# Performance work log

Measured on AMD Instinct MI355X. Metric: run time of the kernel, lower is better.

## Reference

```python
import jax, jax.numpy as jnp
import numpy as np

L, B, T, C = 4, 4, 2048, 1024
FFN = 4 * C
STD = 0.02
EPS = 1e-5
NEG_INF = -1e38


def setup_inputs() -> dict:
    key = jax.random.key(0)
    ks = jax.random.split(key, 18)
    n = lambda k, shape, s=STD: jax.random.normal(k, shape, jnp.float32) * s
    u = lambda k, shape: jax.random.uniform(k, shape, jnp.float32)
    return {
        "x": jax.random.normal(ks[0], (B, T, C), jnp.float32),
        "ln1_w": jnp.ones((L, C), jnp.float32),
        "tm_mix_k": u(ks[1], (L, 1, 1, C)),
        "tm_mix_v": u(ks[2], (L, 1, 1, C)),
        "tm_mix_r": u(ks[3], (L, 1, 1, C)),
        "tm_k_w": n(ks[4], (L, C, C)),
        "tm_v_w": n(ks[5], (L, C, C)),
        "tm_r_w": n(ks[6], (L, C, C)),
        "tm_o_w": n(ks[7], (L, C, C)),
        # time_decay in [-5, 1] like RWKV decay_speed init; w = -exp(time_decay)
        "time_decay": u(ks[8], (L, C)) * 6.0 - 5.0,
        "time_first": jnp.log(0.3).astype(jnp.float32) + 0.5 * jax.random.normal(ks[9], (L, C), jnp.float32),
        "ln2_w": jnp.ones((L, C), jnp.float32),
        "cm_mix_k": u(ks[10], (L, 1, 1, C)),
        "cm_mix_r": u(ks[11], (L, 1, 1, C)),
        "cm_k_w": n(ks[12], (L, FFN, C)),
        "cm_v_w": n(ks[13], (L, C, FFN)),
        "cm_r_w": n(ks[14], (L, C, C)),
        "lnf_w": jnp.ones((C,), jnp.float32),
    }


def layer_norm(x, w):
    mu = jnp.mean(x, axis=-1, keepdims=True)
    var = jnp.mean(jnp.square(x - mu), axis=-1, keepdims=True)
    return (x - mu) * jax.lax.rsqrt(var + EPS) * w


def time_shift(x):
    # ZeroPad2d((0,0,1,-1)): shift sequence right by one, zero at t=0
    return jnp.pad(x, ((0, 0), (1, 0), (0, 0)))[:, :-1]


def wkv_scan(k, v, time_decay, time_first):
    # k, v: [B, T, C]; numerically-stabilized linear WKV recurrence over T
    w = -jnp.exp(time_decay)  # [C]
    u = time_first            # [C]
    zeros = jnp.zeros(k.shape[::2], k.dtype)  # [B, C]

    def step(carry, kv):
        num, den, mx = carry
        kt, vt = kv
        max_out = jnp.maximum(mx, kt + u)
        e1 = jnp.exp(mx - max_out)
        e2 = jnp.exp(kt + u - max_out)
        out = (e1 * num + e2 * vt) / (e1 * den + e2)
        max_st = jnp.maximum(mx + w, kt)
        e1 = jnp.exp(mx + w - max_st)
        e2 = jnp.exp(kt - max_st)
        return (e1 * num + e2 * vt, e1 * den + e2, max_st), out

    init = (zeros, zeros, jnp.full_like(zeros, NEG_INF))
    _, out = jax.lax.scan(step, init, (k.swapaxes(0, 1), v.swapaxes(0, 1)))
    return out.swapaxes(0, 1)  # [B, T, C]


def reference(x, ln1_w, tm_mix_k, tm_mix_v, tm_mix_r, tm_k_w, tm_v_w, tm_r_w, tm_o_w,
              time_decay, time_first, ln2_w, cm_mix_k, cm_mix_r, cm_k_w, cm_v_w, cm_r_w, lnf_w):
    n_layer = ln1_w.shape[0]
    for l in range(n_layer):
        # --- TimeMixing ---
        h = layer_norm(x, ln1_w[l])
        prev = time_shift(h)
        k = jnp.einsum('btc,oc->bto', h * tm_mix_k[l] + prev * (1 - tm_mix_k[l]), tm_k_w[l])
        v = jnp.einsum('btc,oc->bto', h * tm_mix_v[l] + prev * (1 - tm_mix_v[l]), tm_v_w[l])
        r = jax.nn.sigmoid(jnp.einsum('btc,oc->bto', h * tm_mix_r[l] + prev * (1 - tm_mix_r[l]), tm_r_w[l]))
        wkv = wkv_scan(k, v, time_decay[l], time_first[l])
        x = x + jnp.einsum('btc,oc->bto', r * wkv, tm_o_w[l])
        # --- ChannelMixing ---
        h = layer_norm(x, ln2_w[l])
        prev = time_shift(h)
        kk = jnp.einsum('btc,fc->btf', h * cm_mix_k[l] + prev * (1 - cm_mix_k[l]), cm_k_w[l])  # [B,T,4C]
        vv = jnp.einsum('btf,of->bto', jnp.square(jax.nn.relu(kk)), cm_v_w[l])
        rr = jax.nn.sigmoid(jnp.einsum('btc,oc->bto', h * cm_mix_r[l] + prev * (1 - cm_mix_r[l]), cm_r_w[l]))
        x = x + rr * vv
    return layer_norm(x, lnf_w)
```

## Files before the change

### kernel.cpp

```cpp
#include <hip/hip_runtime.h>
#include <hip/hip_bf16.h>


#define LNUM 4
#define BSZ  4
#define TSZ  2048
#define CSZ  1024
#define FFND 4096
#define MROWS (BSZ*TSZ)
#define EPSF 1e-5f

typedef __hip_bfloat16 bf16;
typedef __bf16 bf16x8 __attribute__((ext_vector_type(8)));
typedef float f32x4 __attribute__((ext_vector_type(4)));

#define BM 128
#define BK 64

#define SCK  64
#define SLEN (TSZ/SCK)

__device__ __forceinline__ void async_copy16(const void* g, void* l) {
    __builtin_amdgcn_global_load_lds((const __attribute__((address_space(1))) void*)g,
                                     (__attribute__((address_space(3))) void*)l, 16, 0, 0);
}

template<int MODE, int TBN>
__launch_bounds__(256)
__global__ void gemm_bt(const bf16* __restrict__ A, const bf16* __restrict__ Bw,
                        void* __restrict__ outp, const bf16* __restrict__ aux,
                        int K, int N)
{
    constexpr int MT  = (TBN == 128) ? 4 : 2;
    constexpr int NBI = TBN / 32;
    __shared__ __align__(16) __bf16 sA[BM*BK];
    __shared__ __align__(16) __bf16 sB[TBN*BK];
    const int tid  = threadIdx.x;
    const int lane = tid & 63;
    const int wid  = tid >> 6;
    const int wmB  = (TBN == 128) ? (wid >> 1) * 64 : wid * 32;
    const int wnB  = (TBN == 128) ? (wid & 1) * 64 : 0;
    const size_t bm0 = (size_t)blockIdx.x * BM;
    const size_t bn0 = (size_t)blockIdx.y * TBN;

    const int lrow8 = lane >> 3;
    const int cbg   = (lane & 7) ^ lrow8;

    const bf16* pA[4]; const bf16* pB[NBI];
#pragma unroll
    for (int i = 0; i < 4; ++i)
        pA[i] = A + (bm0 + (i*4 + wid)*8 + lrow8) * (size_t)K + cbg*8;
#pragma unroll
    for (int i = 0; i < NBI; ++i)
        pB[i] = Bw + (bn0 + (i*4 + wid)*8 + lrow8) * (size_t)K + cbg*8;

    f32x4 acc[MT][4];
#pragma unroll
    for (int a = 0; a < MT; ++a)
#pragma unroll
        for (int b = 0; b < 4; ++b) acc[a][b] = (f32x4){0.f,0.f,0.f,0.f};

    const int q   = lane >> 4;
    const int rlo = lane & 15;

    const int ktiles = K / BK;
    for (int kt = 0; kt < ktiles; ++kt) {
#pragma unroll
        for (int i = 0; i < 4; ++i) {
            async_copy16(pA[i], &sA[(i*4 + wid)*8*BK]);
            pA[i] += BK;
        }
#pragma unroll
        for (int i = 0; i < NBI; ++i) {
            async_copy16(pB[i], &sB[(i*4 + wid)*8*BK]);
            pB[i] += BK;
        }
        __syncthreads();
#pragma unroll
        for (int ks = 0; ks < 2; ++ks) {
            bf16x8 aF[MT], bF[4];
#pragma unroll
            for (int mt = 0; mt < MT; ++mt) {
                const int r  = wmB + mt*16 + rlo;
                const int cb = (ks*4 + q) ^ (r & 7);
                aF[mt] = *(const bf16x8*)&sA[r*BK + cb*8];
            }
#pragma unroll
            for (int nt = 0; nt < 4; ++nt) {
                const int r  = wnB + nt*16 + rlo;
                const int cb = (ks*4 + q) ^ (r & 7);
                bF[nt] = *(const bf16x8*)&sB[r*BK + cb*8];
            }
#pragma unroll
            for (int mt = 0; mt < MT; ++mt)
#pragma unroll
                for (int nt = 0; nt < 4; ++nt)
                    acc[mt][nt] = __builtin_amdgcn_mfma_f32_16x16x32_bf16(
                        aF[mt], bF[nt], acc[mt][nt], 0, 0, 0);
        }
        __syncthreads();
    }

#pragma unroll
    for (int mt = 0; mt < MT; ++mt) {
#pragma unroll
        for (int nt = 0; nt < 4; ++nt) {
            const size_t col = bn0 + wnB + nt*16 + rlo;
#pragma unroll
            for (int i = 0; i < 4; ++i) {
                const size_t row = bm0 + wmB + mt*16 + q*4 + i;
                const size_t idx = row * (size_t)N + col;
                const float v = acc[mt][nt][i];
                if (MODE == 2) {
                    ((float*)outp)[idx] += v;
                } else if (MODE == 3) {
                    const float t = fmaxf(v, 0.f);
                    ((bf16*)outp)[idx] = __float2bfloat16(t*t);
                } else if (MODE == 4) {
                    ((bf16*)outp)[idx] = __float2bfloat16(1.f/(1.f+__expf(-v)));
                } else if (MODE == 6) {
                    ((float*)outp)[idx] = ((const float*)aux)[idx] + v;
                } else {
                    ((float*)outp)[idx] += (float)aux[idx] * v;
                }
            }
        }
    }
}

__launch_bounds__(256)
__global__ void gemm_kvr(const bf16* __restrict__ A0, const bf16* __restrict__ A1,
                         const bf16* __restrict__ A2,
                         const bf16* __restrict__ W0, const bf16* __restrict__ W1,
                         const bf16* __restrict__ W2,
                         bf16* __restrict__ O0, bf16* __restrict__ O1,
                         bf16* __restrict__ O2)
{
    constexpr int TBN = 64, MT = 2, NBI = 2, K = CSZ, N = CSZ;
    const int z = blockIdx.z;
    const bf16* A  = (z == 0) ? A0 : (z == 1) ? A1 : A2;
    const bf16* Bw = (z == 0) ? W0 : (z == 1) ? W1 : W2;
    bf16* outp     = (z == 0) ? O0 : (z == 1) ? O1 : O2;

    __shared__ __align__(16) __bf16 sA[BM*BK];
    __shared__ __align__(16) __bf16 sB[TBN*BK];
    const int tid  = threadIdx.x;
    const int lane = tid & 63;
    const int wid  = tid >> 6;
    const int wmB  = wid * 32;
    const size_t bm0 = (size_t)blockIdx.x * BM;
    const size_t bn0 = (size_t)blockIdx.y * TBN;

    const int lrow8 = lane >> 3;
    const int cbg   = (lane & 7) ^ lrow8;

    const bf16* pA[4]; const bf16* pB[NBI];
#pragma unroll
    for (int i = 0; i < 4; ++i)
        pA[i] = A + (bm0 + (i*4 + wid)*8 + lrow8) * (size_t)K + cbg*8;
#pragma unroll
    for (int i = 0; i < NBI; ++i)
        pB[i] = Bw + (bn0 + (i*4 + wid)*8 + lrow8) * (size_t)K + cbg*8;

    f32x4 acc[MT][4];
#pragma unroll
    for (int a = 0; a < MT; ++a)
#pragma unroll
        for (int b = 0; b < 4; ++b) acc[a][b] = (f32x4){0.f,0.f,0.f,0.f};

    const int q   = lane >> 4;
    const int rlo = lane & 15;

    for (int kt = 0; kt < K/BK; ++kt) {
#pragma unroll
        for (int i = 0; i < 4; ++i) {
            async_copy16(pA[i], &sA[(i*4 + wid)*8*BK]);
            pA[i] += BK;
        }
#pragma unroll
        for (int i = 0; i < NBI; ++i) {
            async_copy16(pB[i], &sB[(i*4 + wid)*8*BK]);
            pB[i] += BK;
        }
        __syncthreads();
#pragma unroll
        for (int ks = 0; ks < 2; ++ks) {
            bf16x8 aF[MT], bF[4];
#pragma unroll
            for (int mt = 0; mt < MT; ++mt) {
                const int r  = wmB + mt*16 + rlo;
                const int cb = (ks*4 + q) ^ (r & 7);
                aF[mt] = *(const bf16x8*)&sA[r*BK + cb*8];
            }
#pragma unroll
            for (int nt = 0; nt < 4; ++nt) {
                const int r  = nt*16 + rlo;
                const int cb = (ks*4 + q) ^ (r & 7);
                bF[nt] = *(const bf16x8*)&sB[r*BK + cb*8];
            }
#pragma unroll
            for (int mt = 0; mt < MT; ++mt)
#pragma unroll
                for (int nt = 0; nt < 4; ++nt)
                    acc[mt][nt] = __builtin_amdgcn_mfma_f32_16x16x32_bf16(
                        aF[mt], bF[nt], acc[mt][nt], 0, 0, 0);
        }
        __syncthreads();
    }

#pragma unroll
    for (int mt = 0; mt < MT; ++mt) {
#pragma unroll
        for (int nt = 0; nt < 4; ++nt) {
            const size_t col = bn0 + nt*16 + rlo;
#pragma unroll
            for (int i = 0; i < 4; ++i) {
                const size_t row = bm0 + wmB + mt*16 + q*4 + i;
                float v = acc[mt][nt][i];
                if (z == 2) v = 1.f/(1.f+__expf(-v));
                ((bf16*)outp)[row * (size_t)N + col] = __float2bfloat16(v);
            }
        }
    }
}

template<int NOUT>
__launch_bounds__(256)
__global__ void ln_mix_kernel(const float* __restrict__ x, const float* __restrict__ lnw,
                              const float* __restrict__ mka, const float* __restrict__ mva,
                              const float* __restrict__ mra,
                              bf16* __restrict__ ok, bf16* __restrict__ ov, bf16* __restrict__ orr)
{
    const int bt  = blockIdx.x;
    const int t   = bt % TSZ;
    const int tid = threadIdx.x;
    const float4 xc = ((const float4*)(x + (size_t)bt*CSZ))[tid];
    float4 xp = {0.f,0.f,0.f,0.f};
    const bool hasp = (t != 0);
    if (hasp) xp = ((const float4*)(x + (size_t)(bt-1)*CSZ))[tid];

    float s0 = xc.x+xc.y+xc.z+xc.w;
    float s1 = xc.x*xc.x+xc.y*xc.y+xc.z*xc.z+xc.w*xc.w;
    float s2 = xp.x+xp.y+xp.z+xp.w;
    float s3 = xp.x*xp.x+xp.y*xp.y+xp.z*xp.z+xp.w*xp.w;
#pragma unroll
    for (int off = 32; off > 0; off >>= 1) {
        s0 += __shfl_down(s0, off); s1 += __shfl_down(s1, off);
        s2 += __shfl_down(s2, off); s3 += __shfl_down(s3, off);
    }
    __shared__ float red[4][4];
    if ((tid & 63) == 0) { const int wq = tid >> 6;
        red[wq][0]=s0; red[wq][1]=s1; red[wq][2]=s2; red[wq][3]=s3; }
    __syncthreads();
    s0 = red[0][0]+red[1][0]+red[2][0]+red[3][0];
    s1 = red[0][1]+red[1][1]+red[2][1]+red[3][1];
    s2 = red[0][2]+red[1][2]+red[2][2]+red[3][2];
    s3 = red[0][3]+red[1][3]+red[2][3]+red[3][3];

    const float inv = 1.f/CSZ;
    const float muC = s0*inv;
    const float rsC = rsqrtf(s1*inv - muC*muC + EPSF);
    const float muP = s2*inv;
    const float rsP = rsqrtf(s3*inv - muP*muP + EPSF);

    const int c4 = tid*4;
    const float4 lw = ((const float4*)lnw)[tid];
    const float4 mk = ((const float4*)mka)[tid];
    const float4 mv = (NOUT >= 2) ? ((const float4*)mva)[tid] : lw;
    const float4 mr = (NOUT >= 3) ? ((const float4*)mra)[tid] : lw;

    float hcv[4] = {(xc.x-muC)*rsC*lw.x, (xc.y-muC)*rsC*lw.y,
                    (xc.z-muC)*rsC*lw.z, (xc.w-muC)*rsC*lw.w};
    float hpv[4];
    if (hasp) {
        hpv[0]=(xp.x-muP)*rsP*lw.x; hpv[1]=(xp.y-muP)*rsP*lw.y;
        hpv[2]=(xp.z-muP)*rsP*lw.z; hpv[3]=(xp.w-muP)*rsP*lw.w;
    } else { hpv[0]=hpv[1]=hpv[2]=hpv[3]=0.f; }
    const float mkv[4]={mk.x,mk.y,mk.z,mk.w};
    const float mvv[4]={mv.x,mv.y,mv.z,mv.w};
    const float mrv[4]={mr.x,mr.y,mr.z,mr.w};

    __align__(8) bf16 o0[4], o1[4], o2[4];
#pragma unroll
    for (int j = 0; j < 4; ++j) {
        o0[j] = __float2bfloat16(hcv[j]*mkv[j] + hpv[j]*(1.f-mkv[j]));
        if (NOUT >= 2) o1[j] = __float2bfloat16(hcv[j]*mvv[j] + hpv[j]*(1.f-mvv[j]));
        if (NOUT >= 3) o2[j] = __float2bfloat16(hcv[j]*mrv[j] + hpv[j]*(1.f-mrv[j]));
    }
    *(uint2*)(ok + (size_t)bt*CSZ + c4) = *(const uint2*)o0;
    if (NOUT >= 2) *(uint2*)(ov  + (size_t)bt*CSZ + c4) = *(const uint2*)o1;
    if (NOUT >= 3) *(uint2*)(orr + (size_t)bt*CSZ + c4) = *(const uint2*)o2;
}

__launch_bounds__(256)
__global__ void wkv_sum_kernel(const bf16* __restrict__ kb, const bf16* __restrict__ vb,
                               const float* __restrict__ td,
                               float* __restrict__ sN, float* __restrict__ sD,
                               float* __restrict__ sM)
{
    const int j  = blockIdx.x;
    const int b  = blockIdx.y >> 2;
    const int cg = blockIdx.y & 3;
    const int c  = cg*256 + threadIdx.x;
    const float w = -__expf(td[c]);

    size_t idx = ((size_t)b*TSZ + j*SLEN)*CSZ + c;
    float num = 0.f, den = 0.f, mx = -1e38f;
    float kt = (float)kb[idx], vt = (float)vb[idx];
    for (int t = 0; t < SLEN; ++t) {
        float kn = 0.f, vn = 0.f;
        if (t + 1 < SLEN) {
            kn = (float)kb[idx + CSZ]; vn = (float)vb[idx + CSZ];
        }
        const float ms = fmaxf(mx + w, kt);
        const float p1 = __expf(mx + w - ms);
        const float p2 = __expf(kt - ms);
        num = p1*num + p2*vt; den = p1*den + p2; mx = ms;
        idx += CSZ; kt = kn; vt = vn;
    }
    const size_t sidx = ((size_t)b*SCK + j)*CSZ + c;
    sN[sidx] = num; sD[sidx] = den; sM[sidx] = mx;
}

__launch_bounds__(256)
__global__ void wkv_out_kernel(const bf16* __restrict__ kb, const bf16* __restrict__ vb,
                               const bf16* __restrict__ rb,
                               const float* __restrict__ td, const float* __restrict__ tf,
                               const float* __restrict__ sN, const float* __restrict__ sD,
                               const float* __restrict__ sM,
                               bf16* __restrict__ outb)
{
    const int j  = blockIdx.x;
    const int b  = blockIdx.y >> 2;
    const int cg = blockIdx.y & 3;
    const int c  = cg*256 + threadIdx.x;
    const float w = -__expf(td[c]);
    const float u = tf[c];
    const float wL = w * (float)SLEN;

    float num = 0.f, den = 0.f, mx = -1e38f;
    size_t pidx = (size_t)b*SCK*CSZ + c;
    for (int jj = 0; jj < j; ++jj) {
        const float nl = sN[pidx], dl = sD[pidx], ml = sM[pidx];
        const float mi = mx + wL;
        const float mo = fmaxf(mi, ml);
        const float e1 = __expf(mi - mo);
        const float e2 = __expf(ml - mo);
        num = e1*num + e2*nl; den = e1*den + e2*dl; mx = mo;
        pidx += CSZ;
    }

    size_t idx = ((size_t)b*TSZ + j*SLEN)*CSZ + c;
    float kt = (float)kb[idx], vt = (float)vb[idx], rt = (float)rb[idx];
    for (int t = 0; t < SLEN; ++t) {
        float kn = 0.f, vn = 0.f, rn = 0.f;
        if (t + 1 < SLEN) {
            kn = (float)kb[idx + CSZ]; vn = (float)vb[idx + CSZ]; rn = (float)rb[idx + CSZ];
        }
        const float ku = kt + u;
        const float mo = fmaxf(mx, ku);
        const float e1 = __expf(mx - mo);
        const float e2 = __expf(ku - mo);
        const float outv = (e1*num + e2*vt) / (e1*den + e2);
        const float ms = fmaxf(mx + w, kt);
        const float p1 = __expf(mx + w - ms);
        const float p2 = __expf(kt - ms);
        num = p1*num + p2*vt; den = p1*den + p2; mx = ms;
        outb[idx] = __float2bfloat16(rt * outv);
        idx += CSZ; kt = kn; vt = vn; rt = rn;
    }
}

__launch_bounds__(256)
__global__ void final_ln_kernel(const float* __restrict__ x, const float* __restrict__ lnw,
                                float* __restrict__ out)
{
    const int bt  = blockIdx.x;
    const int tid = threadIdx.x;
    const float4 xc = ((const float4*)(x + (size_t)bt*CSZ))[tid];
    float s0 = xc.x+xc.y+xc.z+xc.w;
    float s1 = xc.x*xc.x+xc.y*xc.y+xc.z*xc.z+xc.w*xc.w;
#pragma unroll
    for (int off = 32; off > 0; off >>= 1) {
        s0 += __shfl_down(s0, off); s1 += __shfl_down(s1, off);
    }
    __shared__ float red[4][2];
    if ((tid & 63) == 0) { red[tid>>6][0] = s0; red[tid>>6][1] = s1; }
    __syncthreads();
    s0 = red[0][0]+red[1][0]+red[2][0]+red[3][0];
    s1 = red[0][1]+red[1][1]+red[2][1]+red[3][1];
    const float inv = 1.f/CSZ;
    const float mu = s0*inv;
    const float rs = rsqrtf(s1*inv - mu*mu + EPSF);
    const float4 lw = ((const float4*)lnw)[tid];
    float4 o;
    o.x = (xc.x-mu)*rs*lw.x; o.y = (xc.y-mu)*rs*lw.y;
    o.z = (xc.z-mu)*rs*lw.z; o.w = (xc.w-mu)*rs*lw.w;
    ((float4*)(out + (size_t)bt*CSZ))[tid] = o;
}

#define N4_CC (CSZ*CSZ/4)
#define N4_FC (FFND*CSZ/4)
__global__ void cvt_weights_kernel(const float* __restrict__ tk, const float* __restrict__ tv,
                                   const float* __restrict__ tr, const float* __restrict__ to,
                                   const float* __restrict__ ck, const float* __restrict__ cv,
                                   const float* __restrict__ cr,
                                   bf16* __restrict__ wk, bf16* __restrict__ wv,
                                   bf16* __restrict__ wr, bf16* __restrict__ wo,
                                   bf16* __restrict__ wck, bf16* __restrict__ wcv,
                                   bf16* __restrict__ wcr)
{
    int i = blockIdx.x * 256 + threadIdx.x;
    const float* s; bf16* d;
    if      (i < 1*N4_CC)          { s = tk; d = wk;  }
    else if (i < 2*N4_CC)          { s = tv; d = wv;  i -= 1*N4_CC; }
    else if (i < 3*N4_CC)          { s = tr; d = wr;  i -= 2*N4_CC; }
    else if (i < 4*N4_CC)          { s = to; d = wo;  i -= 3*N4_CC; }
    else if (i < 4*N4_CC+N4_FC)    { s = ck; d = wck; i -= 4*N4_CC; }
    else if (i < 4*N4_CC+2*N4_FC)  { s = cv; d = wcv; i -= 4*N4_CC+N4_FC; }
    else                           { s = cr; d = wcr; i -= 4*N4_CC+2*N4_FC; }
    const float4 f = ((const float4*)s)[i];
    __align__(8) bf16 o[4] = {__float2bfloat16(f.x), __float2bfloat16(f.y),
                              __float2bfloat16(f.z), __float2bfloat16(f.w)};
    ((uint2*)d)[i] = *(const uint2*)o;
}
#define CVT_TOTAL4 (4*N4_CC + 2*N4_FC + N4_CC)

static constexpr size_t SZ_XF32 = (size_t)MROWS*CSZ*4;
static constexpr size_t SZ_ABF  = (size_t)MROWS*CSZ*2;
static constexpr size_t OFF_X   = 0;
static constexpr size_t OFF_XK  = OFF_X  + SZ_XF32;
static constexpr size_t OFF_XV  = OFF_XK + SZ_ABF;
static constexpr size_t OFF_XR  = OFF_XV + SZ_ABF;
static constexpr size_t OFF_K   = OFF_XR + SZ_ABF;
static constexpr size_t OFF_V   = OFF_K  + SZ_ABF;
static constexpr size_t OFF_R   = OFF_V  + SZ_ABF;
static constexpr size_t OFF_KK  = OFF_R  + SZ_ABF;
static constexpr size_t OFF_W   = OFF_KK + (size_t)MROWS*FFND*2;
static constexpr size_t OFF_WK  = OFF_W;
static constexpr size_t OFF_WV  = OFF_WK + (size_t)CSZ*CSZ*2;
static constexpr size_t OFF_WR  = OFF_WV + (size_t)CSZ*CSZ*2;
static constexpr size_t OFF_WO  = OFF_WR + (size_t)CSZ*CSZ*2;
static constexpr size_t OFF_WCK = OFF_WO + (size_t)CSZ*CSZ*2;
static constexpr size_t OFF_WCV = OFF_WCK + (size_t)FFND*CSZ*2;
static constexpr size_t OFF_WCR = OFF_WCV + (size_t)CSZ*FFND*2;

static constexpr size_t SZ_SUM  = (size_t)BSZ*SCK*CSZ*4;

extern "C" void kernel_launch(void* const* d_in, const int* in_sizes, int n_in,
                              void* d_out, int out_size, void* d_ws, size_t ws_size,
                              hipStream_t stream)
{
    const float* xin   = (const float*)d_in[0];
    const float* ln1w  = (const float*)d_in[1];
    const float* tmixk = (const float*)d_in[2];
    const float* tmixv = (const float*)d_in[3];
    const float* tmixr = (const float*)d_in[4];
    const float* tkw   = (const float*)d_in[5];
    const float* tvw   = (const float*)d_in[6];
    const float* trw   = (const float*)d_in[7];
    const float* tow   = (const float*)d_in[8];
    const float* tdec  = (const float*)d_in[9];
    const float* tfst  = (const float*)d_in[10];
    const float* ln2w  = (const float*)d_in[11];
    const float* cmixk = (const float*)d_in[12];
    const float* cmixr = (const float*)d_in[13];
    const float* ckw   = (const float*)d_in[14];
    const float* cvw   = (const float*)d_in[15];
    const float* crw   = (const float*)d_in[16];
    const float* lnfw  = (const float*)d_in[17];

    char* ws = (char*)d_ws;
    float* xres = (float*)(ws + OFF_X);
    bf16* xk  = (bf16*)(ws + OFF_XK);
    bf16* xv  = (bf16*)(ws + OFF_XV);
    bf16* xr  = (bf16*)(ws + OFF_XR);
    bf16* kb  = (bf16*)(ws + OFF_K);
    bf16* vb  = (bf16*)(ws + OFF_V);
    bf16* rb  = (bf16*)(ws + OFF_R);
    bf16* kkb = (bf16*)(ws + OFF_KK);
    bf16* rwkv = xk;
    bf16* rr  = (bf16*)(ws + OFF_K);
    float* sN  = (float*)(ws + OFF_KK);
    float* sD  = (float*)(ws + OFF_KK + SZ_SUM);
    float* sM  = (float*)(ws + OFF_KK + 2*SZ_SUM);
    bf16* wk  = (bf16*)(ws + OFF_WK);
    bf16* wv  = (bf16*)(ws + OFF_WV);
    bf16* wr  = (bf16*)(ws + OFF_WR);
    bf16* wo  = (bf16*)(ws + OFF_WO);
    bf16* wck = (bf16*)(ws + OFF_WCK);
    bf16* wcv = (bf16*)(ws + OFF_WCV);
    bf16* wcr = (bf16*)(ws + OFF_WCR);

    const dim3 blk(256);
    const dim3 gKVR(MROWS/BM, CSZ/64, 3);
    const dim3 gC64(MROWS/BM, CSZ/64);
    const dim3 gF(MROWS/BM, FFND/128);
    const dim3 gScan(SCK, BSZ*4);

    for (int l = 0; l < LNUM; ++l) {
        const size_t oC  = (size_t)l*CSZ;
        const size_t oCC = (size_t)l*CSZ*CSZ;
        const size_t oFC = (size_t)l*FFND*CSZ;
        cvt_weights_kernel<<<CVT_TOTAL4/256, blk, 0, stream>>>(
            tkw + oCC, tvw + oCC, trw + oCC, tow + oCC,
            ckw + oFC, cvw + oFC, crw + oCC,
            wk, wv, wr, wo, wck, wcv, wcr);

        ln_mix_kernel<3><<<MROWS, blk, 0, stream>>>(l == 0 ? xin : xres, ln1w + oC,
            tmixk + oC, tmixv + oC, tmixr + oC, xk, xv, xr);
        gemm_kvr<<<gKVR, blk, 0, stream>>>(xk, xv, xr, wk, wv, wr, kb, vb, rb);
        wkv_sum_kernel<<<gScan, blk, 0, stream>>>(kb, vb, tdec + oC, sN, sD, sM);
        wkv_out_kernel<<<gScan, blk, 0, stream>>>(kb, vb, rb, tdec + oC, tfst + oC,
            sN, sD, sM, rwkv);
        if (l == 0) {
            gemm_bt<6,64><<<gC64, blk, 0, stream>>>(rwkv, wo, xres,
                (const bf16*)xin, CSZ, CSZ);
        } else {
            gemm_bt<2,64><<<gC64, blk, 0, stream>>>(rwkv, wo, xres, nullptr, CSZ, CSZ);
        }

        ln_mix_kernel<2><<<MROWS, blk, 0, stream>>>(xres, ln2w + oC,
            cmixk + oC, cmixr + oC, nullptr, xk, xv, nullptr);
        gemm_bt<3,128><<<gF, blk, 0, stream>>>(xk, wck, kkb, nullptr, CSZ, FFND);
        gemm_bt<4,64><<<gC64, blk, 0, stream>>>(xv, wcr, rr, nullptr, CSZ, CSZ);
        gemm_bt<5,64><<<gC64, blk, 0, stream>>>(kkb, wcv, xres, rr, FFND, CSZ);
    }
    final_ln_kernel<<<MROWS, blk, 0, stream>>>(xres, lnfw, (float*)d_out);
}
```

Baseline: 1.737 ms.

## Widen KVR tiles, fuse channel-mix K/R GEMMs, split-K the value GEMM

The K/V/R projection GEMM now uses 128x128 tiles, with each wave computing a 64x64 sub-tile, which raises the number of MFMAs per shared-memory load. The channel-mix key and receptance GEMMs are merged into one launch whose grid covers both output ranges. The FFN value GEMM is split two ways along K using a new LDK stride and blockIdx.z, and partial sums are added into the residual with float atomics. Atomic accumulation adds traffic and makes the summation order nondeterministic, and the larger tiles leave fewer blocks in the KVR grid.

```diff
diff --git a/kernel.cpp b/kernel.cpp
--- a/kernel.cpp
+++ b/kernel.cpp
@@ -29,7 +29,7 @@
 __launch_bounds__(256)
 __global__ void gemm_bt(const bf16* __restrict__ A, const bf16* __restrict__ Bw,
                         void* __restrict__ outp, const bf16* __restrict__ aux,
-                        int K, int N)
+                        int K, int LDK, int N)
 {
     constexpr int MT  = (TBN == 128) ? 4 : 2;
     constexpr int NBI = TBN / 32;
@@ -42,6 +42,7 @@
     const int wnB  = (TBN == 128) ? (wid & 1) * 64 : 0;
     const size_t bm0 = (size_t)blockIdx.x * BM;
     const size_t bn0 = (size_t)blockIdx.y * TBN;
+    const size_t koff = (size_t)blockIdx.z * K;
 
     const int lrow8 = lane >> 3;
     const int cbg   = (lane & 7) ^ lrow8;
@@ -49,10 +50,10 @@
     const bf16* pA[4]; const bf16* pB[NBI];
 #pragma unroll
     for (int i = 0; i < 4; ++i)
-        pA[i] = A + (bm0 + (i*4 + wid)*8 + lrow8) * (size_t)K + cbg*8;
+        pA[i] = A + (bm0 + (i*4 + wid)*8 + lrow8) * (size_t)LDK + koff + cbg*8;
 #pragma unroll
     for (int i = 0; i < NBI; ++i)
-        pB[i] = Bw + (bn0 + (i*4 + wid)*8 + lrow8) * (size_t)K + cbg*8;
+        pB[i] = Bw + (bn0 + (i*4 + wid)*8 + lrow8) * (size_t)LDK + koff + cbg*8;
 
     f32x4 acc[MT][4];
 #pragma unroll
@@ -120,6 +121,8 @@
                     ((bf16*)outp)[idx] = __float2bfloat16(1.f/(1.f+__expf(-v)));
                 } else if (MODE == 6) {
                     ((float*)outp)[idx] = ((const float*)aux)[idx] + v;
+                } else if (MODE == 7) {
+                    unsafeAtomicAdd(&((float*)outp)[idx], (float)aux[idx] * v);
                 } else {
                     ((float*)outp)[idx] += (float)aux[idx] * v;
                 }
@@ -136,20 +139,21 @@
                          bf16* __restrict__ O0, bf16* __restrict__ O1,
                          bf16* __restrict__ O2)
 {
-    constexpr int TBN = 64, MT = 2, NBI = 2, K = CSZ, N = CSZ;
+    constexpr int MT = 4, NBI = 4, K = CSZ, N = CSZ;
     const int z = blockIdx.z;
     const bf16* A  = (z == 0) ? A0 : (z == 1) ? A1 : A2;
     const bf16* Bw = (z == 0) ? W0 : (z == 1) ? W1 : W2;
     bf16* outp     = (z == 0) ? O0 : (z == 1) ? O1 : O2;
 
     __shared__ __align__(16) __bf16 sA[BM*BK];
-    __shared__ __align__(16) __bf16 sB[TBN*BK];
+    __shared__ __align__(16) __bf16 sB[128*BK];
     const int tid  = threadIdx.x;
     const int lane = tid & 63;
     const int wid  = tid >> 6;
-    const int wmB  = wid * 32;
+    const int wmB  = (wid >> 1) * 64;
+    const int wnB  = (wid & 1) * 64;
     const size_t bm0 = (size_t)blockIdx.x * BM;
-    const size_t bn0 = (size_t)blockIdx.y * TBN;
+    const size_t bn0 = (size_t)blockIdx.y * 128;
 
     const int lrow8 = lane >> 3;
     const int cbg   = (lane & 7) ^ lrow8;
@@ -194,7 +198,7 @@
             }
 #pragma unroll
             for (int nt = 0; nt < 4; ++nt) {
-                const int r  = nt*16 + rlo;
+                const int r  = wnB + nt*16 + rlo;
                 const int cb = (ks*4 + q) ^ (r & 7);
                 bF[nt] = *(const bf16x8*)&sB[r*BK + cb*8];
             }
@@ -212,13 +216,110 @@
     for (int mt = 0; mt < MT; ++mt) {
 #pragma unroll
         for (int nt = 0; nt < 4; ++nt) {
-            const size_t col = bn0 + nt*16 + rlo;
+            const size_t col = bn0 + wnB + nt*16 + rlo;
 #pragma unroll
             for (int i = 0; i < 4; ++i) {
                 const size_t row = bm0 + wmB + mt*16 + q*4 + i;
                 float v = acc[mt][nt][i];
                 if (z == 2) v = 1.f/(1.f+__expf(-v));
                 ((bf16*)outp)[row * (size_t)N + col] = __float2bfloat16(v);
+            }
+        }
+    }
+}
+
+__launch_bounds__(256)
+__global__ void gemm_cmkr(const bf16* __restrict__ Ak, const bf16* __restrict__ Ar,
+                          const bf16* __restrict__ Wk, const bf16* __restrict__ Wr,
+                          bf16* __restrict__ Ok, bf16* __restrict__ Or)
+{
+    constexpr int MT = 4, NBI = 4, K = CSZ;
+    const bool isk = (blockIdx.y < FFND/128);
+    const bf16* A  = isk ? Ak : Ar;
+    const bf16* Bw = isk ? Wk : Wr;
+    bf16* outp     = isk ? Ok : Or;
+    const int N    = isk ? FFND : CSZ;
+    const size_t bn0 = (size_t)(isk ? blockIdx.y : blockIdx.y - FFND/128) * 128;
+
+    __shared__ __align__(16) __bf16 sA[BM*BK];
+    __shared__ __align__(16) __bf16 sB[128*BK];
+    const int tid  = threadIdx.x;
+    const int lane = tid & 63;
+    const int wid  = tid >> 6;
+    const int wmB  = (wid >> 1) * 64;
+    const int wnB  = (wid & 1) * 64;
+    const size_t bm0 = (size_t)blockIdx.x * BM;
+
+    const int lrow8 = lane >> 3;
+    const int cbg   = (lane & 7) ^ lrow8;
+
+    const bf16* pA[4]; const bf16* pB[NBI];
+#pragma unroll
+    for (int i = 0; i < 4; ++i)
+        pA[i] = A + (bm0 + (i*4 + wid)*8 + lrow8) * (size_t)K + cbg*8;
+#pragma unroll
+    for (int i = 0; i < NBI; ++i)
+        pB[i] = Bw + (bn0 + (i*4 + wid)*8 + lrow8) * (size_t)K + cbg*8;
+
+    f32x4 acc[MT][4];
+#pragma unroll
+    for (int a = 0; a < MT; ++a)
+#pragma unroll
+        for (int b = 0; b < 4; ++b) acc[a][b] = (f32x4){0.f,0.f,0.f,0.f};
+
+    const int q   = lane >> 4;
+    const int rlo = lane & 15;
+
+    for (int kt = 0; kt < K/BK; ++kt) {
+#pragma unroll
+        for (int i = 0; i < 4; ++i) {
+            async_copy16(pA[i], &sA[(i*4 + wid)*8*BK]);
+            pA[i] += BK;
+        }
+#pragma unroll
+        for (int i = 0; i < NBI; ++i) {
+            async_copy16(pB[i], &sB[(i*4 + wid)*8*BK]);
+            pB[i] += BK;
+        }
+        __syncthreads();
+#pragma unroll
+        for (int ks = 0; ks < 2; ++ks) {
+            bf16x8 aF[MT], bF[4];
+#pragma unroll
+            for (int mt = 0; mt < MT; ++mt) {
+                const int r  = wmB + mt*16 + rlo;
+                const int cb = (ks*4 + q) ^ (r & 7);
+                aF[mt] = *(const bf16x8*)&sA[r*BK + cb*8];
+            }
+#pragma unroll
+            for (int nt = 0; nt < 4; ++nt) {
+                const int r  = wnB + nt*16 + rlo;
+                const int cb = (ks*4 + q) ^ (r & 7);
+                bF[nt] = *(const bf16x8*)&sB[r*BK + cb*8];
+            }
+#pragma unroll
+            for (int mt = 0; mt < MT; ++mt)
+#pragma unroll
+                for (int nt = 0; nt < 4; ++nt)
+                    acc[mt][nt] = __builtin_amdgcn_mfma_f32_16x16x32_bf16(
+                        aF[mt], bF[nt], acc[mt][nt], 0, 0, 0);
+        }
+        __syncthreads();
+    }
+
+#pragma unroll
+    for (int mt = 0; mt < MT; ++mt) {
+#pragma unroll
+        for (int nt = 0; nt < 4; ++nt) {
+            const size_t col = bn0 + wnB + nt*16 + rlo;
+#pragma unroll
+            for (int i = 0; i < 4; ++i) {
+                const size_t row = bm0 + wmB + mt*16 + q*4 + i;
+                const float v = acc[mt][nt][i];
+                float o;
+                if (isk) { const float t = fmaxf(v, 0.f); o = t*t; }
+                else     { o = 1.f/(1.f+__expf(-v)); }
+                ((bf16*)outp)[row * (size_t)N + col] = __float2bfloat16(o);
             }
         }
     }
@@ -493,9 +594,10 @@
     bf16* wcr = (bf16*)(ws + OFF_WCR);
 
     const dim3 blk(256);
-    const dim3 gKVR(MROWS/BM, CSZ/64, 3);
+    const dim3 gKVR(MROWS/BM, CSZ/128, 3);
     const dim3 gC64(MROWS/BM, CSZ/64);
-    const dim3 gF(MROWS/BM, FFND/128);
+    const dim3 gCMKR(MROWS/BM, FFND/128 + CSZ/128);
+    const dim3 gCMV(MROWS/BM, CSZ/128, 2);
     const dim3 gScan(SCK, BSZ*4);
 
     for (int l = 0; l < LNUM; ++l) {
@@ -515,16 +617,17 @@
             sN, sD, sM, rwkv);
         if (l == 0) {
             gemm_bt<6,64><<<gC64, blk, 0, stream>>>(rwkv, wo, xres,
-                (const bf16*)xin, CSZ, CSZ);
+                (const bf16*)xin, CSZ, CSZ, CSZ);
         } else {
-            gemm_bt<2,64><<<gC64, blk, 0, stream>>>(rwkv, wo, xres, nullptr, CSZ, CSZ);
+            gemm_bt<2,64><<<gC64, blk, 0, stream>>>(rwkv, wo, xres, nullptr,
+                CSZ, CSZ, CSZ);
         }
 
         ln_mix_kernel<2><<<MROWS, blk, 0, stream>>>(xres, ln2w + oC,
             cmixk + oC, cmixr + oC, nullptr, xk, xv, nullptr);
-        gemm_bt<3,128><<<gF, blk, 0, stream>>>(xk, wck, kkb, nullptr, CSZ, FFND);
-        gemm_bt<4,64><<<gC64, blk, 0, stream>>>(xv, wcr, rr, nullptr, CSZ, CSZ);
-        gemm_bt<5,64><<<gC64, blk, 0, stream>>>(kkb, wcv, xres, rr, FFND, CSZ);
+        gemm_cmkr<<<gCMKR, blk, 0, stream>>>(xk, xv, wck, wcr, kkb, rr);
+        gemm_bt<7,128><<<gCMV, blk, 0, stream>>>(kkb, wcv, xres, rr,
+            FFND/2, FFND, CSZ);
     }
     final_ln_kernel<<<MROWS, blk, 0, stream>>>(xres, lnfw, (float*)d_out);
 }
```

New measurement: 1.870 ms. +7.7%, slower.
